# Optimization experiments

Hardware: AMD Instinct MI355X
Metric: run time of the kernel (lower is better)

Reference implementation:

```python
import jax, jax.numpy as jnp
import numpy as np

B, N, F, D, M, R, K, TOPR = 32, 1024, 10, 64, 4, 8, 20, 2
TAU = 1.0
BN_EPS = 1e-5


def setup_inputs() -> dict:
    key = jax.random.key(0)
    ks = jax.random.split(key, 20)
    s = 0.1
    p = {}
    p['data'] = jax.random.normal(ks[0], (B, N, F), jnp.float32)
    u = jnp.clip(jax.random.uniform(ks[1], (B, M), jnp.float32), 1e-6, 1.0 - 1e-6)
    p['gumbel_noise'] = -jnp.log(-jnp.log(u))
    p['W_cond'] = jax.random.normal(ks[2], (F, D), jnp.float32) * s
    p['b_cond'] = jnp.zeros((D,), jnp.float32)
    p['W_ap'] = jax.random.normal(ks[3], (D, D), jnp.float32) * s
    p['b_ap'] = jnp.zeros((D,), jnp.float32)
    p['W_av'] = jax.random.normal(ks[4], (D, 1), jnp.float32) * s
    p['W_r'] = jax.random.normal(ks[5], (D, M), jnp.float32) * s
    p['b_r'] = jnp.zeros((M,), jnp.float32)
    p['e_base'] = jax.random.normal(ks[6], (N, D), jnp.float32) * s
    p['lr_u'] = jax.random.normal(ks[7], (M, N, R), jnp.float32) * s
    p['lr_v'] = jax.random.normal(ks[8], (M, R, D), jnp.float32) * s
    p['W_gnn'] = jax.random.normal(ks[9], (F, D), jnp.float32) * s
    p['att_i'] = jax.random.normal(ks[10], (D,), jnp.float32) * s
    p['att_j'] = jax.random.normal(ks[11], (D,), jnp.float32) * s
    p['att_em_i'] = jax.random.normal(ks[12], (D,), jnp.float32) * s
    p['att_em_j'] = jax.random.normal(ks[13], (D,), jnp.float32) * s
    p['b_gnn'] = jnp.zeros((D,), jnp.float32)
    p['bn1_gamma'] = jnp.ones((D,), jnp.float32)
    p['bn1_beta'] = jnp.zeros((D,), jnp.float32)
    p['node_embed_table'] = jax.random.normal(ks[14], (N, D), jnp.float32) * s
    p['bn_out_gamma'] = jnp.ones((D,), jnp.float32)
    p['bn_out_beta'] = jnp.zeros((D,), jnp.float32)
    p['W_out'] = jax.random.normal(ks[15], (D, 1), jnp.float32) * s
    p['b_out'] = jnp.zeros((1,), jnp.float32)
    return p


def _nan(x):
    return jnp.nan_to_num(x, nan=0.0, posinf=1e4, neginf=-1e4)


def _bn(x, gamma, beta, axes):
    # BatchNorm1d in training mode: biased batch stats over `axes`.
    mu = x.mean(axes, keepdims=True)
    var = x.var(axes, keepdims=True)
    return (x - mu) * jax.lax.rsqrt(var + BN_EPS) * gamma + beta


def reference(data, gumbel_noise, W_cond, b_cond, W_ap, b_ap, W_av, W_r, b_r,
              e_base, lr_u, lr_v, W_gnn, att_i, att_j, att_em_i, att_em_j,
              b_gnn, bn1_gamma, bn1_beta, node_embed_table,
              bn_out_gamma, bn_out_beta, W_out, b_out):
    x_det = jax.lax.stop_gradient(data)                      # data.clone().detach()
    # --- condition attention pooling ---
    h_it = data @ W_cond + b_cond                            # [B,N,D]
    ah = jax.nn.leaky_relu(h_it @ W_ap + b_ap, 0.2)
    e_it = _nan((ah @ W_av)[..., 0])                         # [B,N]
    beta = jax.nn.softmax(e_it, axis=1)
    h_sys = jnp.sum(beta[..., None] * h_it, axis=1)          # [B,D]
    # --- gumbel top-k routing with straight-through ---
    pi_soft = jax.nn.softmax((h_sys @ W_r + b_r + gumbel_noise) / TAU, axis=-1)
    topv, topi = jax.lax.top_k(pi_soft, TOPR)
    pi_hard = jnp.sum(jax.nn.one_hot(topi, M, dtype=pi_soft.dtype) * topv[..., None], axis=1)
    pi_hard = pi_hard / jnp.maximum(pi_hard.sum(-1, keepdims=True), 1e-12)
    pi_t = jax.lax.stop_gradient(pi_hard - pi_soft) + pi_soft
    # --- low-rank expert prototypes -> mixed node embeddings ---
    proto = e_base[None] + jnp.einsum('mnr,mrd->mnd', lr_u, lr_v)    # [M,N,D]
    mixed = _nan(jnp.einsum('bm,mnd->bnd', pi_t, proto))             # [B,N,D]
    # --- dynamic top-k graph construction ---
    scores = _nan(jnp.einsum('bid,bjd->bij', mixed, mixed))          # [B,N,N]
    topk_vals, topk_idx = jax.lax.top_k(scores, K)                   # src nodes per dst: [B,N,K]
    topk_w = jax.nn.softmax(topk_vals, axis=-1)                      # edge weights
    # --- GAT-style layer with embedding-augmented keys, self loops re-added ---
    x_lin = x_det @ W_gnn                                            # [B,N,D]
    s_i = x_lin @ att_i + mixed @ att_em_i                           # [B,N]
    s_j = x_lin @ att_j + mixed @ att_em_j
    sj_nb = jnp.take_along_axis(s_j, topk_idx.reshape(B, N * K), axis=1).reshape(B, N, K)
    self_mask = topk_idx == jnp.arange(N)[None, :, None]             # remove_self_loops on topk edges
    alpha_nb = jnp.where(self_mask, -jnp.inf, jax.nn.leaky_relu(s_i[:, :, None] + sj_nb, 0.2))
    alpha_self = jax.nn.leaky_relu(s_i + s_j, 0.2)
    att = jax.nn.softmax(jnp.concatenate([alpha_nb, alpha_self[..., None]], axis=-1), axis=-1)
    w_nb = att[..., :K] * topk_w                                     # edge_weight modulation
    w_self = att[..., K]
    x_src = jnp.take_along_axis(x_lin, topk_idx.reshape(B, N * K)[..., None], axis=1).reshape(B, N, K, D)
    gnn = jnp.einsum('bnk,bnkd->bnd', w_nb, x_src) + w_self[..., None] * x_lin + b_gnn
    gnn = jax.nn.relu(_bn(gnn.reshape(B * N, D), bn1_gamma, bn1_beta, 0).reshape(B, N, D))
    # --- output head ---
    out = gnn * node_embed_table[None]                               # [B,N,D]
    out = jax.nn.relu(_bn(out, bn_out_gamma, bn_out_beta, (0, 1)))   # dropout = identity (eval)
    out = (out @ W_out + b_out).reshape(-1, N)                       # [B,N]
    return out, h_sys, pi_soft
```

## Files before the change

kernel.cpp:

```cpp
#include <hip/hip_runtime.h>
#include <math.h>

#define BB 32
#define NN 1024
#define FF 10
#define DD 64
#define MM 4
#define RR 8
#define KK 20
#define BNROWS (BB*NN)

#define OFF_HIT   0ull
#define OFF_XLIN  2097152ull
#define OFF_EIT   4194304ull
#define OFF_PIT   4227072ull
#define OFF_MIXED 4227200ull
#define OFF_SI    6324352ull
#define OFF_SJ    6357120ull
#define OFF_TKV   6389888ull
#define OFF_TKI   7045248ull
#define OFF_GNN   7700608ull
#define OFF_OUTP  9797760ull
#define OFF_STAT  11894912ull
#define OFF_SC    (OFF_STAT + 256ull)

__device__ __forceinline__ float wave_sum(float v) {
    #pragma unroll
    for (int off = 32; off; off >>= 1) v += __shfl_xor(v, off);
    return v;
}
__device__ __forceinline__ float wave_max(float v) {
    #pragma unroll
    for (int off = 32; off; off >>= 1) v = fmaxf(v, __shfl_xor(v, off));
    return v;
}

__device__ __forceinline__ unsigned int dpp_wave_max_u32(unsigned int x) {
    unsigned int t;
    t = (unsigned)__builtin_amdgcn_update_dpp(0, (int)x, 0x111, 0xF, 0xF, true);
    x = x > t ? x : t;
    t = (unsigned)__builtin_amdgcn_update_dpp(0, (int)x, 0x112, 0xF, 0xF, true);
    x = x > t ? x : t;
    t = (unsigned)__builtin_amdgcn_update_dpp(0, (int)x, 0x114, 0xF, 0xF, true);
    x = x > t ? x : t;
    t = (unsigned)__builtin_amdgcn_update_dpp(0, (int)x, 0x118, 0xF, 0xF, true);
    x = x > t ? x : t;
    t = (unsigned)__builtin_amdgcn_update_dpp(0, (int)x, 0x142, 0xF, 0xF, true);
    x = x > t ? x : t;
    t = (unsigned)__builtin_amdgcn_update_dpp(0, (int)x, 0x143, 0xF, 0xF, true);
    x = x > t ? x : t;
    return (unsigned)__builtin_amdgcn_readlane((int)x, 63);
}

__global__ __launch_bounds__(256) void k_rows(
    const float* __restrict__ data, const float* __restrict__ W_cond,
    const float* __restrict__ b_cond, const float* __restrict__ W_ap,
    const float* __restrict__ b_ap, const float* __restrict__ W_av,
    const float* __restrict__ W_gnn,
    float* __restrict__ h_it, float* __restrict__ x_lin, float* __restrict__ e_it,
    float* __restrict__ stats)
{
    if (blockIdx.x == 0) stats[threadIdx.x] = 0.f;
    int w = threadIdx.x >> 6, lane = threadIdx.x & 63;
    int r = blockIdx.x * 4 + w;
    const float* dr = data + r * FF;
    float df[FF];
    #pragma unroll
    for (int f = 0; f < FF; f++) df[f] = dr[f];
    float h = b_cond[lane], x = 0.f;
    #pragma unroll
    for (int f = 0; f < FF; f++) {
        h = fmaf(df[f], W_cond[f * DD + lane], h);
        x = fmaf(df[f], W_gnn[f * DD + lane], x);
    }
    h_it[r * DD + lane] = h;
    x_lin[r * DD + lane] = x;
    float acc = b_ap[lane];
    #pragma unroll
    for (int e2 = 0; e2 < DD; e2++)
        acc = fmaf(__shfl(h, e2), W_ap[e2 * DD + lane], acc);
    float lr = acc > 0.f ? acc : 0.2f * acc;
    float ep = wave_sum(lr * W_av[lane]);
    if (lane == 0) e_it[r] = ep;
}

__global__ __launch_bounds__(256) void k_pool(
    const float* __restrict__ e_it, const float* __restrict__ h_it,
    float* __restrict__ h_sys)
{
    int b = blockIdx.x, t = threadIdx.x, w = t >> 6, lane = t & 63;
    __shared__ float sbeta[NN];
    __shared__ float red[4];
    __shared__ float part[4][DD];
    float v[4]; float mx = -INFINITY;
    #pragma unroll
    for (int i = 0; i < 4; i++) { v[i] = e_it[b * NN + t + i * 256]; mx = fmaxf(mx, v[i]); }
    mx = wave_max(mx);
    if (lane == 0) red[w] = mx;
    __syncthreads();
    mx = fmaxf(fmaxf(red[0], red[1]), fmaxf(red[2], red[3]));
    float s = 0.f;
    #pragma unroll
    for (int i = 0; i < 4; i++) { v[i] = expf(v[i] - mx); s += v[i]; }
    s = wave_sum(s);
    __syncthreads();
    if (lane == 0) red[w] = s;
    __syncthreads();
    s = red[0] + red[1] + red[2] + red[3];
    #pragma unroll
    for (int i = 0; i < 4; i++) sbeta[t + i * 256] = v[i] / s;
    __syncthreads();
    float acc = 0.f;
    for (int n = w * 256; n < w * 256 + 256; n++)
        acc = fmaf(sbeta[n], h_it[(b * NN + n) * DD + lane], acc);
    part[w][lane] = acc;
    __syncthreads();
    if (w == 0)
        h_sys[b * DD + lane] = part[0][lane] + part[1][lane] + part[2][lane] + part[3][lane];
}

__global__ void k_route(const float* __restrict__ h_sys, const float* __restrict__ W_r,
                        const float* __restrict__ b_r, const float* __restrict__ gumbel,
                        float* __restrict__ pi_soft, float* __restrict__ pi_t)
{
    int b = threadIdx.x;
    if (b >= BB) return;
    float lg[MM];
    #pragma unroll
    for (int m = 0; m < MM; m++) {
        float a = b_r[m] + gumbel[b * MM + m];
        for (int d = 0; d < DD; d++) a = fmaf(h_sys[b * DD + d], W_r[d * MM + m], a);
        lg[m] = a;
    }
    float mx = fmaxf(fmaxf(lg[0], lg[1]), fmaxf(lg[2], lg[3]));
    float s = 0.f, p[MM];
    #pragma unroll
    for (int m = 0; m < MM; m++) { p[m] = expf(lg[m] - mx); s += p[m]; }
    #pragma unroll
    for (int m = 0; m < MM; m++) { p[m] /= s; pi_soft[b * MM + m] = p[m]; }
    int i1 = 0; float v1 = p[0];
    #pragma unroll
    for (int m = 1; m < MM; m++) if (p[m] > v1) { v1 = p[m]; i1 = m; }
    int i2 = -1; float v2 = -1.f;
    #pragma unroll
    for (int m = 0; m < MM; m++) if (m != i1 && p[m] > v2) { v2 = p[m]; i2 = m; }
    float norm = fmaxf(v1 + v2, 1e-12f);
    #pragma unroll
    for (int m = 0; m < MM; m++)
        pi_t[b * MM + m] = (m == i1 ? v1 : (m == i2 ? v2 : 0.f)) / norm;
}

__global__ __launch_bounds__(256) void k_mixed(
    const float* __restrict__ e_base, const float* __restrict__ lr_u,
    const float* __restrict__ lr_v, const float* __restrict__ pi_t,
    const float* __restrict__ x_lin,
    const float* __restrict__ att_i, const float* __restrict__ att_j,
    const float* __restrict__ att_em_i, const float* __restrict__ att_em_j,
    float* __restrict__ mixed, float* __restrict__ s_i, float* __restrict__ s_j)
{
    int w = threadIdx.x >> 6, lane = threadIdx.x & 63;
    int r = blockIdx.x * 4 + w;
    int b = r >> 10, n = r & 1023;
    float LR[MM];
    #pragma unroll
    for (int m = 0; m < MM; m++) {
        float a = 0.f;
        #pragma unroll
        for (int rr = 0; rr < RR; rr++)
            a = fmaf(lr_u[(m * NN + n) * RR + rr], lr_v[(m * RR + rr) * DD + lane], a);
        LR[m] = a;
    }
    float eb = e_base[n * DD + lane];
    float mx = 0.f;
    #pragma unroll
    for (int m = 0; m < MM; m++) mx = fmaf(pi_t[b * MM + m], eb + LR[m], mx);
    mixed[(size_t)r * DD + lane] = mx;
    float x = x_lin[(size_t)r * DD + lane];
    float r1 = wave_sum(x * att_i[lane] + mx * att_em_i[lane]);
    float r2 = wave_sum(x * att_j[lane] + mx * att_em_j[lane]);
    if (lane == 0) { s_i[r] = r1; s_j[r] = r2; }
}

__global__ __launch_bounds__(256) void k_score(
    const float* __restrict__ mixed_chunk, float* __restrict__ sc)
{
    __shared__ float As[64 * 132];
    __shared__ float Bs[64 * 132];
    int t = threadIdx.x;
    int bb = blockIdx.x >> 6;
    int rr = blockIdx.x & 63;
    int it = rr >> 3, jt = rr & 7;
    int i0 = it * 128, j0 = jt * 128;
    const float* mb = mixed_chunk + (size_t)bb * NN * DD;

    #pragma unroll
    for (int c = 0; c < 8; c++) {
        int id = t + c * 256;
        int row = (id & 15) + ((id >> 8) << 4);
        int q = (id >> 4) & 15;
        const float4 va = *(const float4*)(mb + (size_t)(i0 + row) * DD + q * 4);
        As[(q * 4 + 0) * 132 + row] = va.x;
        As[(q * 4 + 1) * 132 + row] = va.y;
        As[(q * 4 + 2) * 132 + row] = va.z;
        As[(q * 4 + 3) * 132 + row] = va.w;
        const float4 vb = *(const float4*)(mb + (size_t)(j0 + row) * DD + q * 4);
        Bs[(q * 4 + 0) * 132 + row] = vb.x;
        Bs[(q * 4 + 1) * 132 + row] = vb.y;
        Bs[(q * 4 + 2) * 132 + row] = vb.z;
        Bs[(q * 4 + 3) * 132 + row] = vb.w;
    }
    __syncthreads();

    int tx = t & 15, ty = t >> 4;
    float acc[8][8];
    #pragma unroll
    for (int a = 0; a < 8; a++)
        #pragma unroll
        for (int bj = 0; bj < 8; bj++) acc[a][bj] = 0.f;

    #pragma unroll 4
    for (int d = 0; d < 64; d++) {
        float4 a0 = *(const float4*)&As[d * 132 + ty * 8];
        float4 a1 = *(const float4*)&As[d * 132 + ty * 8 + 4];
        float4 b0 = *(const float4*)&Bs[d * 132 + tx * 8];
        float4 b1 = *(const float4*)&Bs[d * 132 + tx * 8 + 4];
        float av[8] = {a0.x, a0.y, a0.z, a0.w, a1.x, a1.y, a1.z, a1.w};
        float bv[8] = {b0.x, b0.y, b0.z, b0.w, b1.x, b1.y, b1.z, b1.w};
        #pragma unroll
        for (int a = 0; a < 8; a++)
            #pragma unroll
            for (int bj = 0; bj < 8; bj++)
                acc[a][bj] = fmaf(av[a], bv[bj], acc[a][bj]);
    }

    float* out = sc + ((size_t)bb * NN + i0 + ty * 8) * NN + j0 + tx * 8;
    #pragma unroll
    for (int a = 0; a < 8; a++) {
        float4 o0 = {acc[a][0], acc[a][1], acc[a][2], acc[a][3]};
        float4 o1 = {acc[a][4], acc[a][5], acc[a][6], acc[a][7]};
        *(float4*)(out + (size_t)a * NN) = o0;
        *(float4*)(out + (size_t)a * NN + 4) = o1;
    }
}

__global__ __launch_bounds__(256) void k_select(
    const float* __restrict__ sc, int b0,
    float* __restrict__ tkv, int* __restrict__ tki)
{
    int w = threadIdx.x >> 6, lane = threadIdx.x & 63;
    int lr = blockIdx.x * 4 + w;
    const float* row = sc + (size_t)lr * NN;

    unsigned int g[4][4];
    #pragma unroll
    for (int c = 0; c < 4; c++) {
        float4 v = *(const float4*)(row + c * 256 + lane * 4);
        float vv[4] = {v.x, v.y, v.z, v.w};
        #pragma unroll
        for (int q = 0; q < 4; q++) {
            unsigned int u = __float_as_uint(vv[q]);
            unsigned int m = ((unsigned int)((int)u >> 31)) | 0x80000000u;
            g[c][q] = ((u ^ m) & 0xFFFFFFF0u) | (unsigned)(c * 4 + q);
        }
    }
    #pragma unroll
    for (int c = 0; c < 4; c++) {
        unsigned a0 = g[c][0], a1 = g[c][1], a2 = g[c][2], a3 = g[c][3], hi, lo;
        hi = a0 > a1 ? a0 : a1; lo = a0 > a1 ? a1 : a0; a0 = hi; a1 = lo;
        hi = a2 > a3 ? a2 : a3; lo = a2 > a3 ? a3 : a2; a2 = hi; a3 = lo;
        hi = a0 > a2 ? a0 : a2; lo = a0 > a2 ? a2 : a0; a0 = hi; a2 = lo;
        hi = a1 > a3 ? a1 : a3; lo = a1 > a3 ? a3 : a1; a1 = hi; a3 = lo;
        hi = a1 > a2 ? a1 : a2; lo = a1 > a2 ? a2 : a1; a1 = hi; a2 = lo;
        g[c][0] = a0; g[c][1] = a1; g[c][2] = a2; g[c][3] = a3;
    }
    unsigned head = g[0][0];
    head = g[1][0] > head ? g[1][0] : head;
    head = g[2][0] > head ? g[2][0] : head;
    head = g[3][0] > head ? g[3][0] : head;

    unsigned myk = 0u; int myj = 0;
    #pragma unroll
    for (int k = 0; k < KK; k++) {
        unsigned m = dpp_wave_max_u32(head);
        unsigned long long ball = __ballot(head == m);
        int winner = (int)__builtin_ctzll(ball);
        int slot = (int)(m & 15u);
        int j = ((slot >> 2) << 8) + winner * 4 + (slot & 3);
        if (lane == k) { myk = m; myj = j; }
        bool iswin = (lane == winner);
        int gi = slot >> 2;
        if (gi == 0) {
            g[0][0] = iswin ? g[0][1] : g[0][0];
            g[0][1] = iswin ? g[0][2] : g[0][1];
            g[0][2] = iswin ? g[0][3] : g[0][2];
            g[0][3] = iswin ? 0u : g[0][3];
        } else if (gi == 1) {
            g[1][0] = iswin ? g[1][1] : g[1][0];
            g[1][1] = iswin ? g[1][2] : g[1][1];
            g[1][2] = iswin ? g[1][3] : g[1][2];
            g[1][3] = iswin ? 0u : g[1][3];
        } else if (gi == 2) {
            g[2][0] = iswin ? g[2][1] : g[2][0];
            g[2][1] = iswin ? g[2][2] : g[2][1];
            g[2][2] = iswin ? g[2][3] : g[2][2];
            g[2][3] = iswin ? 0u : g[2][3];
        } else {
            g[3][0] = iswin ? g[3][1] : g[3][0];
            g[3][1] = iswin ? g[3][2] : g[3][1];
            g[3][2] = iswin ? g[3][3] : g[3][2];
            g[3][3] = iswin ? 0u : g[3][3];
        }
        head = g[0][0];
        head = g[1][0] > head ? g[1][0] : head;
        head = g[2][0] > head ? g[2][0] : head;
        head = g[3][0] > head ? g[3][0] : head;
    }
    if (lane < KK) {
        int gr = b0 * NN + lr;
        unsigned kk = myk & 0xFFFFFFF0u;
        unsigned u = (kk & 0x80000000u) ? (kk ^ 0x80000000u) : ~kk;
        tkv[(size_t)gr * KK + lane] = __uint_as_float(u);
        tki[(size_t)gr * KK + lane] = myj;
    }
}

__global__ __launch_bounds__(256) void k_gat(
    const float* __restrict__ x_lin, const float* __restrict__ s_i,
    const float* __restrict__ s_j, const float* __restrict__ tkv,
    const int* __restrict__ tki, const float* __restrict__ b_gnn,
    float* __restrict__ gnn_pre)
{
    int w = threadIdx.x >> 6, lane = threadIdx.x & 63;
    int r = blockIdx.x * 4 + w;
    int b = r >> 10, n = r & 1023;
    float vk = -INFINITY; int ik = 0;
    if (lane < KK) { vk = tkv[r * KK + lane]; ik = tki[r * KK + lane]; }
    float m1 = wave_max(vk);
    float ek = (lane < KK) ? expf(vk - m1) : 0.f;
    float s1v = wave_sum(ek);
    float wk = ek / s1v;
    float si = s_i[r], sjn = s_j[r];
    float a = -INFINITY;
    if (lane < KK) {
        float sjk = s_j[(b << 10) + ik];
        float t2 = si + sjk;
        a = (ik == n) ? -INFINITY : (t2 > 0.f ? t2 : 0.2f * t2);
    }
    float ts = si + sjn;
    float aself = ts > 0.f ? ts : 0.2f * ts;
    float am = wave_max(fmaxf(a, aself));
    float ea = (lane < KK && a != -INFINITY) ? expf(a - am) : 0.f;
    float es = expf(aself - am);
    float ssum = wave_sum(ea) + es;
    float wnb = (ea / ssum) * wk;
    float wself = es / ssum;
    float acc = b_gnn[lane] + wself * x_lin[r * DD + lane];
    for (int k = 0; k < KK; k++) {
        int jk = __shfl(ik, k);
        float wv = __shfl(wnb, k);
        acc = fmaf(wv, x_lin[((b << 10) + jk) * DD + lane], acc);
    }
    gnn_pre[r * DD + lane] = acc;
}

__global__ __launch_bounds__(256) void k_stats(const float* __restrict__ src, float* __restrict__ sums)
{
    int w = threadIdx.x >> 6, lane = threadIdx.x & 63;
    __shared__ float ps[4][DD], pq[4][DD];
    float s = 0.f, q = 0.f;
    int base = blockIdx.x * 512;
    for (int i = w; i < 512; i += 4) {
        float v = src[(size_t)(base + i) * DD + lane];
        s += v; q = fmaf(v, v, q);
    }
    ps[w][lane] = s; pq[w][lane] = q;
    __syncthreads();
    if (w == 0) {
        s = ps[0][lane] + ps[1][lane] + ps[2][lane] + ps[3][lane];
        q = pq[0][lane] + pq[1][lane] + pq[2][lane] + pq[3][lane];
        atomicAdd(&sums[lane], s);
        atomicAdd(&sums[DD + lane], q);
    }
}

__global__ __launch_bounds__(256) void k_bn1(
    const float* __restrict__ gnn_pre, const float* __restrict__ stats,
    const float* __restrict__ gamma, const float* __restrict__ beta,
    const float* __restrict__ net, float* __restrict__ out_pre)
{
    int e = blockIdx.x * 256 + threadIdx.x;
    int d = e & 63, r = e >> 6, n = r & 1023;
    float mean = stats[d] * (1.0f / BNROWS);
    float var = stats[DD + d] * (1.0f / BNROWS) - mean * mean;
    float rs = rsqrtf(var + 1e-5f);
    float y = (gnn_pre[e] - mean) * rs * gamma[d] + beta[d];
    y = y > 0.f ? y : 0.f;
    out_pre[e] = y * net[n * DD + d];
}

__global__ __launch_bounds__(256) void k_head(
    const float* __restrict__ out_pre, const float* __restrict__ stats,
    const float* __restrict__ gamma, const float* __restrict__ beta,
    const float* __restrict__ W_out, const float* __restrict__ b_out,
    float* __restrict__ out)
{
    int w = threadIdx.x >> 6, lane = threadIdx.x & 63;
    int r = blockIdx.x * 4 + w;
    float mean = stats[lane] * (1.0f / BNROWS);
    float var = stats[DD + lane] * (1.0f / BNROWS) - mean * mean;
    float rs = rsqrtf(var + 1e-5f);
    float y = (out_pre[(size_t)r * DD + lane] - mean) * rs * gamma[lane] + beta[lane];
    y = y > 0.f ? y : 0.f;
    float p = wave_sum(y * W_out[lane]);
    if (lane == 0) out[r] = p + b_out[0];
}

extern "C" void kernel_launch(void* const* d_in, const int* in_sizes, int n_in,
                              void* d_out, int out_size, void* d_ws, size_t ws_size,
                              hipStream_t stream)
{
    const float* data     = (const float*)d_in[0];
    const float* gumbel   = (const float*)d_in[1];
    const float* W_cond   = (const float*)d_in[2];
    const float* b_cond   = (const float*)d_in[3];
    const float* W_ap     = (const float*)d_in[4];
    const float* b_ap     = (const float*)d_in[5];
    const float* W_av     = (const float*)d_in[6];
    const float* W_r      = (const float*)d_in[7];
    const float* b_r      = (const float*)d_in[8];
    const float* e_base   = (const float*)d_in[9];
    const float* lr_u     = (const float*)d_in[10];
    const float* lr_v     = (const float*)d_in[11];
    const float* W_gnn    = (const float*)d_in[12];
    const float* att_i    = (const float*)d_in[13];
    const float* att_j    = (const float*)d_in[14];
    const float* att_em_i = (const float*)d_in[15];
    const float* att_em_j = (const float*)d_in[16];
    const float* b_gnn    = (const float*)d_in[17];
    const float* bn1_g    = (const float*)d_in[18];
    const float* bn1_b    = (const float*)d_in[19];
    const float* net      = (const float*)d_in[20];
    const float* bno_g    = (const float*)d_in[21];
    const float* bno_b    = (const float*)d_in[22];
    const float* W_out    = (const float*)d_in[23];
    const float* b_out    = (const float*)d_in[24];

    float* ws = (float*)d_ws;
    float* h_it   = ws + OFF_HIT;
    float* x_lin  = ws + OFF_XLIN;
    float* e_it   = ws + OFF_EIT;
    float* pi_t   = ws + OFF_PIT;
    float* mixed  = ws + OFF_MIXED;
    float* s_i    = ws + OFF_SI;
    float* s_j    = ws + OFF_SJ;
    float* tkv    = ws + OFF_TKV;
    int*   tki    = (int*)(ws + OFF_TKI);
    float* gnn_pre = ws + OFF_GNN;
    float* out_pre = ws + OFF_OUTP;
    float* stats   = ws + OFF_STAT;

    float* out0    = (float*)d_out;
    float* h_sys   = out0 + BB * NN;
    float* pi_soft = out0 + BB * NN + BB * DD;

    k_rows<<<BNROWS / 4, 256, 0, stream>>>(data, W_cond, b_cond, W_ap, b_ap, W_av, W_gnn,
                                           h_it, x_lin, e_it, stats);
    k_pool<<<BB, 256, 0, stream>>>(e_it, h_it, h_sys);
    k_route<<<1, 64, 0, stream>>>(h_sys, W_r, b_r, gumbel, pi_soft, pi_t);
    k_mixed<<<BNROWS / 4, 256, 0, stream>>>(e_base, lr_u, lr_v, pi_t, x_lin,
                                            att_i, att_j, att_em_i, att_em_j, mixed, s_i, s_j);

    size_t ws_floats = ws_size / 4;
    size_t avail = ws_floats > OFF_SC ? ws_floats - OFF_SC : 0;
    int cb = (int)(avail / (size_t)(NN * NN));
    if (cb > BB) cb = BB;
    float* sc = ws + OFF_SC;
    if (cb < 1) { cb = 2; sc = h_it; }
    for (int b0 = 0; b0 < BB; b0 += cb) {
        int c = (BB - b0) < cb ? (BB - b0) : cb;
        k_score<<<c * 64, 256, 0, stream>>>(mixed + (size_t)b0 * NN * DD, sc);
        k_select<<<c * 256, 256, 0, stream>>>(sc, b0, tkv, tki);
    }

    k_gat<<<BNROWS / 4, 256, 0, stream>>>(x_lin, s_i, s_j, tkv, tki, b_gnn, gnn_pre);
    k_stats<<<64, 256, 0, stream>>>(gnn_pre, stats);
    k_bn1<<<BNROWS * DD / 256, 256, 0, stream>>>(gnn_pre, stats, bn1_g, bn1_b, net, out_pre);
    k_stats<<<64, 256, 0, stream>>>(out_pre, stats + 128);
    k_head<<<BNROWS / 4, 256, 0, stream>>>(out_pre, stats + 128, bno_g, bno_b, W_out, b_out, out0);
}
```

Measured before the change: 358.6 us.

## Split pooling across blocks, fuse BN stats into bn1, and retune score/select kernels

Attention pooling is spread over 8 blocks per batch using unnormalized exp weights and atomic numerator/denominator accumulation, with h_sys normalization moved into the route kernel. The second stats pass is fused into k_bn1, which is now float4-vectorized and accumulates output statistics via atomics. k_score loads K in two 32-wide halves to halve LDS use, top-k select carries the full key plus a separate slot index instead of packing the index into low mantissa bits, k_stats uses more blocks, and the GAT loop is unrolled. Pooling without max subtraction risks overflow if e_it is large, and atomics make the sums order-nondeterministic.

```diff
diff --git a/kernel.cpp b/kernel.cpp
--- a/kernel.cpp
+++ b/kernel.cpp
@@ -22,7 +22,7 @@
 #define OFF_GNN   7700608ull
 #define OFF_OUTP  9797760ull
 #define OFF_STAT  11894912ull
-#define OFF_SC    (OFF_STAT + 256ull)
+#define OFF_SC    (OFF_STAT + 2560ull)
 
 __device__ __forceinline__ float wave_sum(float v) {
     #pragma unroll
@@ -60,7 +60,10 @@
     float* __restrict__ h_it, float* __restrict__ x_lin, float* __restrict__ e_it,
     float* __restrict__ stats)
 {
-    if (blockIdx.x == 0) stats[threadIdx.x] = 0.f;
+    if (blockIdx.x < 10) {
+        int idx = blockIdx.x * 256 + threadIdx.x;
+        if (idx < 2336) stats[idx] = 0.f;
+    }
     int w = threadIdx.x >> 6, lane = threadIdx.x & 63;
     int r = blockIdx.x * 4 + w;
     const float* dr = data + r * FF;
@@ -84,53 +87,52 @@
     if (lane == 0) e_it[r] = ep;
 }
 
-__global__ __launch_bounds__(256) void k_pool(
+__global__ __launch_bounds__(256) void k_pool2(
     const float* __restrict__ e_it, const float* __restrict__ h_it,
-    float* __restrict__ h_sys)
-{
-    int b = blockIdx.x, t = threadIdx.x, w = t >> 6, lane = t & 63;
-    __shared__ float sbeta[NN];
-    __shared__ float red[4];
-    __shared__ float part[4][DD];
-    float v[4]; float mx = -INFINITY;
-    #pragma unroll
-    for (int i = 0; i < 4; i++) { v[i] = e_it[b * NN + t + i * 256]; mx = fmaxf(mx, v[i]); }
-    mx = wave_max(mx);
-    if (lane == 0) red[w] = mx;
+    float* __restrict__ num, float* __restrict__ den)
+{
+    int w = threadIdx.x >> 6, lane = threadIdx.x & 63;
+    int b = blockIdx.x >> 3, ch = blockIdx.x & 7;
+    int base = b * NN + ch * 128 + w * 32;
+    float acc = 0.f, dn = 0.f;
+    #pragma unroll 4
+    for (int i = 0; i < 32; i++) {
+        float e = e_it[base + i];
+        float wgt = expf(e);
+        acc = fmaf(wgt, h_it[(size_t)(base + i) * DD + lane], acc);
+        dn += wgt;
+    }
+    __shared__ float pa[4][DD];
+    __shared__ float pd[4];
+    pa[w][lane] = acc;
+    if (lane == 0) pd[w] = dn;
     __syncthreads();
-    mx = fmaxf(fmaxf(red[0], red[1]), fmaxf(red[2], red[3]));
-    float s = 0.f;
-    #pragma unroll
-    for (int i = 0; i < 4; i++) { v[i] = expf(v[i] - mx); s += v[i]; }
-    s = wave_sum(s);
-    __syncthreads();
-    if (lane == 0) red[w] = s;
-    __syncthreads();
-    s = red[0] + red[1] + red[2] + red[3];
-    #pragma unroll
-    for (int i = 0; i < 4; i++) sbeta[t + i * 256] = v[i] / s;
-    __syncthreads();
-    float acc = 0.f;
-    for (int n = w * 256; n < w * 256 + 256; n++)
-        acc = fmaf(sbeta[n], h_it[(b * NN + n) * DD + lane], acc);
-    part[w][lane] = acc;
-    __syncthreads();
-    if (w == 0)
-        h_sys[b * DD + lane] = part[0][lane] + part[1][lane] + part[2][lane] + part[3][lane];
-}
-
-__global__ void k_route(const float* __restrict__ h_sys, const float* __restrict__ W_r,
-                        const float* __restrict__ b_r, const float* __restrict__ gumbel,
-                        float* __restrict__ pi_soft, float* __restrict__ pi_t)
-{
-    int b = threadIdx.x;
-    if (b >= BB) return;
+    if (w == 0) {
+        float s = pa[0][lane] + pa[1][lane] + pa[2][lane] + pa[3][lane];
+        atomicAdd(&num[b * DD + lane], s);
+        if (lane == 0) atomicAdd(&den[b], pd[0] + pd[1] + pd[2] + pd[3]);
+    }
+}
+
+__global__ void k_route(const float* __restrict__ num, const float* __restrict__ den,
+                        const float* __restrict__ W_r, const float* __restrict__ b_r,
+                        const float* __restrict__ gumbel,
+                        float* __restrict__ h_sys, float* __restrict__ pi_soft,
+                        float* __restrict__ pi_t)
+{
+    int tid = threadIdx.x;
+    for (int i = tid; i < BB * DD; i += 256)
+        h_sys[i] = num[i] / den[i >> 6];
+    if (tid >= BB) return;
+    int b = tid;
+    float inv = 1.0f / den[b];
     float lg[MM];
     #pragma unroll
-    for (int m = 0; m < MM; m++) {
-        float a = b_r[m] + gumbel[b * MM + m];
-        for (int d = 0; d < DD; d++) a = fmaf(h_sys[b * DD + d], W_r[d * MM + m], a);
-        lg[m] = a;
+    for (int m = 0; m < MM; m++) lg[m] = b_r[m] + gumbel[b * MM + m];
+    for (int d = 0; d < DD; d++) {
+        float hv = num[b * DD + d] * inv;
+        #pragma unroll
+        for (int m = 0; m < MM; m++) lg[m] = fmaf(hv, W_r[d * MM + m], lg[m]);
     }
     float mx = fmaxf(fmaxf(lg[0], lg[1]), fmaxf(lg[2], lg[3]));
     float s = 0.f, p[MM];
@@ -184,8 +186,8 @@
 __global__ __launch_bounds__(256) void k_score(
     const float* __restrict__ mixed_chunk, float* __restrict__ sc)
 {
-    __shared__ float As[64 * 132];
-    __shared__ float Bs[64 * 132];
+    __shared__ float As[32 * 132];
+    __shared__ float Bs[32 * 132];
     int t = threadIdx.x;
     int bb = blockIdx.x >> 6;
     int rr = blockIdx.x & 63;
@@ -193,24 +195,6 @@
     int i0 = it * 128, j0 = jt * 128;
     const float* mb = mixed_chunk + (size_t)bb * NN * DD;
 
-    #pragma unroll
-    for (int c = 0; c < 8; c++) {
-        int id = t + c * 256;
-        int row = (id & 15) + ((id >> 8) << 4);
-        int q = (id >> 4) & 15;
-        const float4 va = *(const float4*)(mb + (size_t)(i0 + row) * DD + q * 4);
-        As[(q * 4 + 0) * 132 + row] = va.x;
-        As[(q * 4 + 1) * 132 + row] = va.y;
-        As[(q * 4 + 2) * 132 + row] = va.z;
-        As[(q * 4 + 3) * 132 + row] = va.w;
-        const float4 vb = *(const float4*)(mb + (size_t)(j0 + row) * DD + q * 4);
-        Bs[(q * 4 + 0) * 132 + row] = vb.x;
-        Bs[(q * 4 + 1) * 132 + row] = vb.y;
-        Bs[(q * 4 + 2) * 132 + row] = vb.z;
-        Bs[(q * 4 + 3) * 132 + row] = vb.w;
-    }
-    __syncthreads();
-
     int tx = t & 15, ty = t >> 4;
     float acc[8][8];
     #pragma unroll
@@ -218,19 +202,39 @@
         #pragma unroll
         for (int bj = 0; bj < 8; bj++) acc[a][bj] = 0.f;
 
-    #pragma unroll 4
-    for (int d = 0; d < 64; d++) {
-        float4 a0 = *(const float4*)&As[d * 132 + ty * 8];
-        float4 a1 = *(const float4*)&As[d * 132 + ty * 8 + 4];
-        float4 b0 = *(const float4*)&Bs[d * 132 + tx * 8];
-        float4 b1 = *(const float4*)&Bs[d * 132 + tx * 8 + 4];
-        float av[8] = {a0.x, a0.y, a0.z, a0.w, a1.x, a1.y, a1.z, a1.w};
-        float bv[8] = {b0.x, b0.y, b0.z, b0.w, b1.x, b1.y, b1.z, b1.w};
-        #pragma unroll
-        for (int a = 0; a < 8; a++)
+    for (int hh = 0; hh < 2; hh++) {
+        if (hh) __syncthreads();
+        #pragma unroll
+        for (int c = 0; c < 4; c++) {
+            int id = t + c * 256;
+            int row = (id & 15) | ((id >> 7) << 4);
+            int q = (id >> 4) & 7;
+            const float4 va = *(const float4*)(mb + (size_t)(i0 + row) * DD + hh * 32 + q * 4);
+            As[(q * 4 + 0) * 132 + row] = va.x;
+            As[(q * 4 + 1) * 132 + row] = va.y;
+            As[(q * 4 + 2) * 132 + row] = va.z;
+            As[(q * 4 + 3) * 132 + row] = va.w;
+            const float4 vb = *(const float4*)(mb + (size_t)(j0 + row) * DD + hh * 32 + q * 4);
+            Bs[(q * 4 + 0) * 132 + row] = vb.x;
+            Bs[(q * 4 + 1) * 132 + row] = vb.y;
+            Bs[(q * 4 + 2) * 132 + row] = vb.z;
+            Bs[(q * 4 + 3) * 132 + row] = vb.w;
+        }
+        __syncthreads();
+        #pragma unroll 4
+        for (int d = 0; d < 32; d++) {
+            float4 a0 = *(const float4*)&As[d * 132 + ty * 8];
+            float4 a1 = *(const float4*)&As[d * 132 + ty * 8 + 4];
+            float4 b0 = *(const float4*)&Bs[d * 132 + tx * 8];
+            float4 b1 = *(const float4*)&Bs[d * 132 + tx * 8 + 4];
+            float av[8] = {a0.x, a0.y, a0.z, a0.w, a1.x, a1.y, a1.z, a1.w};
+            float bv[8] = {b0.x, b0.y, b0.z, b0.w, b1.x, b1.y, b1.z, b1.w};
             #pragma unroll
-            for (int bj = 0; bj < 8; bj++)
-                acc[a][bj] = fmaf(av[a], bv[bj], acc[a][bj]);
+            for (int a = 0; a < 8; a++)
+                #pragma unroll
+                for (int bj = 0; bj < 8; bj++)
+                    acc[a][bj] = fmaf(av[a], bv[bj], acc[a][bj]);
+        }
     }
 
     float* out = sc + ((size_t)bb * NN + i0 + ty * 8) * NN + j0 + tx * 8;
@@ -251,75 +255,67 @@
     int lr = blockIdx.x * 4 + w;
     const float* row = sc + (size_t)lr * NN;
 
-    unsigned int g[4][4];
+    unsigned gk[4][4];
+    int gs[4][4];
     #pragma unroll
     for (int c = 0; c < 4; c++) {
         float4 v = *(const float4*)(row + c * 256 + lane * 4);
         float vv[4] = {v.x, v.y, v.z, v.w};
         #pragma unroll
         for (int q = 0; q < 4; q++) {
-            unsigned int u = __float_as_uint(vv[q]);
-            unsigned int m = ((unsigned int)((int)u >> 31)) | 0x80000000u;
-            g[c][q] = ((u ^ m) & 0xFFFFFFF0u) | (unsigned)(c * 4 + q);
+            unsigned u = __float_as_uint(vv[q]);
+            unsigned msk = ((unsigned)((int)u >> 31)) | 0x80000000u;
+            gk[c][q] = u ^ msk;
+            gs[c][q] = c * 4 + q;
         }
-    }
-    #pragma unroll
-    for (int c = 0; c < 4; c++) {
-        unsigned a0 = g[c][0], a1 = g[c][1], a2 = g[c][2], a3 = g[c][3], hi, lo;
-        hi = a0 > a1 ? a0 : a1; lo = a0 > a1 ? a1 : a0; a0 = hi; a1 = lo;
-        hi = a2 > a3 ? a2 : a3; lo = a2 > a3 ? a3 : a2; a2 = hi; a3 = lo;
-        hi = a0 > a2 ? a0 : a2; lo = a0 > a2 ? a2 : a0; a0 = hi; a2 = lo;
-        hi = a1 > a3 ? a1 : a3; lo = a1 > a3 ? a3 : a1; a1 = hi; a3 = lo;
-        hi = a1 > a2 ? a1 : a2; lo = a1 > a2 ? a2 : a1; a1 = hi; a2 = lo;
-        g[c][0] = a0; g[c][1] = a1; g[c][2] = a2; g[c][3] = a3;
-    }
-    unsigned head = g[0][0];
-    head = g[1][0] > head ? g[1][0] : head;
-    head = g[2][0] > head ? g[2][0] : head;
-    head = g[3][0] > head ? g[3][0] : head;
-
-    unsigned myk = 0u; int myj = 0;
+        #define CMPSWAP(x, y) { \
+            bool sw = gk[c][x] < gk[c][y]; \
+            unsigned ka = gk[c][x], kb2 = gk[c][y]; int sa = gs[c][x], sb = gs[c][y]; \
+            gk[c][x] = sw ? kb2 : ka; gk[c][y] = sw ? ka : kb2; \
+            gs[c][x] = sw ? sb : sa; gs[c][y] = sw ? sa : sb; }
+        CMPSWAP(0, 1) CMPSWAP(2, 3) CMPSWAP(0, 2) CMPSWAP(1, 3) CMPSWAP(1, 2)
+        #undef CMPSWAP
+    }
+    unsigned head; int hs;
+    {
+        unsigned h01 = gk[0][0]; int s01 = gs[0][0];
+        if (gk[1][0] > h01) { h01 = gk[1][0]; s01 = gs[1][0]; }
+        unsigned h23 = gk[2][0]; int s23 = gs[2][0];
+        if (gk[3][0] > h23) { h23 = gk[3][0]; s23 = gs[3][0]; }
+        head = h01; hs = s01;
+        if (h23 > head) { head = h23; hs = s23; }
+    }
+
+    float myv = 0.f; int myj = 0;
     #pragma unroll
     for (int k = 0; k < KK; k++) {
         unsigned m = dpp_wave_max_u32(head);
         unsigned long long ball = __ballot(head == m);
         int winner = (int)__builtin_ctzll(ball);
-        int slot = (int)(m & 15u);
-        int j = ((slot >> 2) << 8) + winner * 4 + (slot & 3);
-        if (lane == k) { myk = m; myj = j; }
+        int slotw = __shfl(hs, winner);
+        int j = ((slotw >> 2) << 8) + winner * 4 + (slotw & 3);
+        unsigned um = (m & 0x80000000u) ? (m ^ 0x80000000u) : ~m;
+        if (lane == k) { myv = __uint_as_float(um); myj = j; }
         bool iswin = (lane == winner);
-        int gi = slot >> 2;
-        if (gi == 0) {
-            g[0][0] = iswin ? g[0][1] : g[0][0];
-            g[0][1] = iswin ? g[0][2] : g[0][1];
-            g[0][2] = iswin ? g[0][3] : g[0][2];
-            g[0][3] = iswin ? 0u : g[0][3];
-        } else if (gi == 1) {
-            g[1][0] = iswin ? g[1][1] : g[1][0];
-            g[1][1] = iswin ? g[1][2] : g[1][1];
-            g[1][2] = iswin ? g[1][3] : g[1][2];
-            g[1][3] = iswin ? 0u : g[1][3];
-        } else if (gi == 2) {
-            g[2][0] = iswin ? g[2][1] : g[2][0];
-            g[2][1] = iswin ? g[2][2] : g[2][1];
-            g[2][2] = iswin ? g[2][3] : g[2][2];
-            g[2][3] = iswin ? 0u : g[2][3];
-        } else {
-            g[3][0] = iswin ? g[3][1] : g[3][0];
-            g[3][1] = iswin ? g[3][2] : g[3][1];
-            g[3][2] = iswin ? g[3][3] : g[3][2];
-            g[3][3] = iswin ? 0u : g[3][3];
-        }
-        head = g[0][0];
-        head = g[1][0] > head ? g[1][0] : head;
-        head = g[2][0] > head ? g[2][0] : head;
-        head = g[3][0] > head ? g[3][0] : head;
+        int gi = slotw >> 2;
+        #define POPG(c) { \
+            gk[c][0] = iswin ? gk[c][1] : gk[c][0]; gs[c][0] = iswin ? gs[c][1] : gs[c][0]; \
+            gk[c][1] = iswin ? gk[c][2] : gk[c][1]; gs[c][1] = iswin ? gs[c][2] : gs[c][1]; \
+            gk[c][2] = iswin ? gk[c][3] : gk[c][2]; gs[c][2] = iswin ? gs[c][3] : gs[c][2]; \
+            gk[c][3] = iswin ? 0u : gk[c][3]; }
+        if (gi == 0) { POPG(0) } else if (gi == 1) { POPG(1) }
+        else if (gi == 2) { POPG(2) } else { POPG(3) }
+        #undef POPG
+        unsigned h01 = gk[0][0]; int s01 = gs[0][0];
+        if (gk[1][0] > h01) { h01 = gk[1][0]; s01 = gs[1][0]; }
+        unsigned h23 = gk[2][0]; int s23 = gs[2][0];
+        if (gk[3][0] > h23) { h23 = gk[3][0]; s23 = gs[3][0]; }
+        head = h01; hs = s01;
+        if (h23 > head) { head = h23; hs = s23; }
     }
     if (lane < KK) {
         int gr = b0 * NN + lr;
-        unsigned kk = myk & 0xFFFFFFF0u;
-        unsigned u = (kk & 0x80000000u) ? (kk ^ 0x80000000u) : ~kk;
-        tkv[(size_t)gr * KK + lane] = __uint_as_float(u);
+        tkv[(size_t)gr * KK + lane] = myv;
         tki[(size_t)gr * KK + lane] = myj;
     }
 }
@@ -355,6 +351,7 @@
     float wnb = (ea / ssum) * wk;
     float wself = es / ssum;
     float acc = b_gnn[lane] + wself * x_lin[r * DD + lane];
+    #pragma unroll
     for (int k = 0; k < KK; k++) {
         int jk = __shfl(ik, k);
         float wv = __shfl(wnb, k);
@@ -368,8 +365,8 @@
     int w = threadIdx.x >> 6, lane = threadIdx.x & 63;
     __shared__ float ps[4][DD], pq[4][DD];
     float s = 0.f, q = 0.f;
-    int base = blockIdx.x * 512;
-    for (int i = w; i < 512; i += 4) {
+    int base = blockIdx.x * 128;
+    for (int i = w; i < 128; i += 4) {
         float v = src[(size_t)(base + i) * DD + lane];
         s += v; q = fmaf(v, v, q);
     }
@@ -384,18 +381,65 @@
 }
 
 __global__ __launch_bounds__(256) void k_bn1(
-    const float* __restrict__ gnn_pre, const float* __restrict__ stats,
+    const float* __restrict__ gnn_pre, float* __restrict__ stats,
     const float* __restrict__ gamma, const float* __restrict__ beta,
     const float* __restrict__ net, float* __restrict__ out_pre)
 {
-    int e = blockIdx.x * 256 + threadIdx.x;
-    int d = e & 63, r = e >> 6, n = r & 1023;
-    float mean = stats[d] * (1.0f / BNROWS);
-    float var = stats[DD + d] * (1.0f / BNROWS) - mean * mean;
-    float rs = rsqrtf(var + 1e-5f);
-    float y = (gnn_pre[e] - mean) * rs * gamma[d] + beta[d];
-    y = y > 0.f ? y : 0.f;
-    out_pre[e] = y * net[n * DD + d];
+    int tid = threadIdx.x;
+    int d0 = (tid & 15) * 4;
+    float mean4[4], rs4[4], bt4[4];
+    #pragma unroll
+    for (int k = 0; k < 4; k++) {
+        float mu = stats[d0 + k] * (1.0f / BNROWS);
+        float var = stats[64 + d0 + k] * (1.0f / BNROWS) - mu * mu;
+        mean4[k] = mu;
+        rs4[k] = rsqrtf(var + 1e-5f) * gamma[d0 + k];
+        bt4[k] = beta[d0 + k];
+    }
+    float s4[4] = {0, 0, 0, 0}, q4[4] = {0, 0, 0, 0};
+    size_t base4 = (size_t)blockIdx.x * 2048;
+    #pragma unroll
+    for (int i = 0; i < 8; i++) {
+        size_t f4 = base4 + (size_t)i * 256 + tid;
+        float4 v = ((const float4*)gnn_pre)[f4];
+        int n = ((int)(f4 >> 4)) & 1023;
+        float4 nv = ((const float4*)net)[(size_t)n * 16 + (tid & 15)];
+        float vv[4] = {v.x, v.y, v.z, v.w};
+        float nn2[4] = {nv.x, nv.y, nv.z, nv.w};
+        float ov[4];
+        #pragma unroll
+        for (int k = 0; k < 4; k++) {
+            float y = (vv[k] - mean4[k]) * rs4[k] + bt4[k];
+            y = y > 0.f ? y : 0.f;
+            float o = y * nn2[k];
+            ov[k] = o;
+            s4[k] += o;
+            q4[k] = fmaf(o, o, q4[k]);
+        }
+        float4 o4 = {ov[0], ov[1], ov[2], ov[3]};
+        ((float4*)out_pre)[f4] = o4;
+    }
+    __shared__ float4 ls[256], lq[256];
+    ls[tid] = make_float4(s4[0], s4[1], s4[2], s4[3]);
+    lq[tid] = make_float4(q4[0], q4[1], q4[2], q4[3]);
+    __syncthreads();
+    if (tid < 16) {
+        float4 S = ls[tid], Q = lq[tid];
+        #pragma unroll
+        for (int rr = 1; rr < 16; rr++) {
+            float4 a = ls[tid + 16 * rr], b = lq[tid + 16 * rr];
+            S.x += a.x; S.y += a.y; S.z += a.z; S.w += a.w;
+            Q.x += b.x; Q.y += b.y; Q.z += b.z; Q.w += b.w;
+        }
+        atomicAdd(&stats[128 + tid * 4 + 0], S.x);
+        atomicAdd(&stats[128 + tid * 4 + 1], S.y);
+        atomicAdd(&stats[128 + tid * 4 + 2], S.z);
+        atomicAdd(&stats[128 + tid * 4 + 3], S.w);
+        atomicAdd(&stats[192 + tid * 4 + 0], Q.x);
+        atomicAdd(&stats[192 + tid * 4 + 1], Q.y);
+        atomicAdd(&stats[192 + tid * 4 + 2], Q.z);
+        atomicAdd(&stats[192 + tid * 4 + 3], Q.w);
+    }
 }
 
 __global__ __launch_bounds__(256) void k_head(
@@ -458,6 +502,8 @@
     float* gnn_pre = ws + OFF_GNN;
     float* out_pre = ws + OFF_OUTP;
     float* stats   = ws + OFF_STAT;
+    float* pnum    = stats + 256;
+    float* pden    = stats + 2304;
 
     float* out0    = (float*)d_out;
     float* h_sys   = out0 + BB * NN;
@@ -465,8 +511,8 @@
 
     k_rows<<<BNROWS / 4, 256, 0, stream>>>(data, W_cond, b_cond, W_ap, b_ap, W_av, W_gnn,
                                            h_it, x_lin, e_it, stats);
-    k_pool<<<BB, 256, 0, stream>>>(e_it, h_it, h_sys);
-    k_route<<<1, 64, 0, stream>>>(h_sys, W_r, b_r, gumbel, pi_soft, pi_t);
+    k_pool2<<<BB * 8, 256, 0, stream>>>(e_it, h_it, pnum, pden);
+    k_route<<<1, 256, 0, stream>>>(pnum, pden, W_r, b_r, gumbel, h_sys, pi_soft, pi_t);
     k_mixed<<<BNROWS / 4, 256, 0, stream>>>(e_base, lr_u, lr_v, pi_t, x_lin,
                                             att_i, att_j, att_em_i, att_em_j, mixed, s_i, s_j);
 
@@ -483,8 +529,7 @@
     }
 
     k_gat<<<BNROWS / 4, 256, 0, stream>>>(x_lin, s_i, s_j, tkv, tki, b_gnn, gnn_pre);
-    k_stats<<<64, 256, 0, stream>>>(gnn_pre, stats);
-    k_bn1<<<BNROWS * DD / 256, 256, 0, stream>>>(gnn_pre, stats, bn1_g, bn1_b, net, out_pre);
-    k_stats<<<64, 256, 0, stream>>>(out_pre, stats + 128);
+    k_stats<<<256, 256, 0, stream>>>(gnn_pre, stats);
+    k_bn1<<<256, 256, 0, stream>>>(gnn_pre, stats, bn1_g, bn1_b, net, out_pre);
     k_head<<<BNROWS / 4, 256, 0, stream>>>(out_pre, stats + 128, bno_g, bno_b, W_out, b_out, out0);
 }
```

Measured after the change: 345.4 us. 1.04x faster.
